# Performance work log

Hardware: AMD Instinct MI355X
Metric: run time of the kernel (lower is better)

Reference implementation:

```python
import jax, jax.numpy as jnp
import numpy as np
import math

N, C, E, K_TOP = 4096, 256, 131072, 32
NEG_SLOPE = 0.2  # GATConv default negative_slope


def _mlp(x, w1, b1, w2, b2):
    # Linear -> relu -> Linear (dropout is identity in eval mode)
    return jax.nn.relu(x @ w1 + b1) @ w2 + b2


def _gat_alpha(x, w, a_src, a_dst, src, dst, n):
    # PyG GATConv attention coefficients (heads=1), softmax over incoming edges per dst
    h = x @ w                                                   # [N,C]
    logits = jax.nn.leaky_relu((h @ a_src)[src] + (h @ a_dst)[dst], NEG_SLOPE)  # [E]
    m = jnp.full((n,), -jnp.inf, dtype=logits.dtype).at[dst].max(logits)
    e = jnp.exp(logits - m[dst])
    s = jax.ops.segment_sum(e, dst, num_segments=n)
    return e / s[dst]                                           # [E]


def _mha_w(x, wq, bq, wk, bk):
    # nn.MultiheadAttention attention weights, heads=1, unbatched [N,C] input
    q = x @ wq + bq
    k = x @ wk + bk
    return jax.nn.softmax((q @ k.T) * (1.0 / math.sqrt(C)), axis=-1)  # [N,N]


def _forward(ae, pe, se,
             ae_w1, ae_b1, ae_w2, ae_b2,
             pe_w1, pe_b1, pe_w2, pe_b2,
             se_w1, se_b1, se_w2, se_b2,
             ae_gw, ae_as, ae_ad,
             pe_gw, pe_as, pe_ad,
             se_gw, se_as, se_ad,
             ae_wq, ae_bq, ae_wk, ae_bk,
             pe_wq, pe_bq, pe_wk, pe_bk,
             se_wq, se_bq, se_wk, se_bk,
             a_l, b_l, c_l, a_g, b_g, c_g,
             w_local, w_global,
             edge_index, K):
    n = ae.shape[0]
    ae = _mlp(ae, ae_w1, ae_b1, ae_w2, ae_b2)
    pe = _mlp(pe, pe_w1, pe_b1, pe_w2, pe_b2)
    se = _mlp(se, se_w1, se_b1, se_w2, se_b2)

    src, dst = edge_index[0], edge_index[1]

    # ---- local branch: fused GAT attention coeffs -> weighted mean aggregation ----
    pa = _gat_alpha(pe, pe_gw, pe_as, pe_ad, src, dst, n)
    sa = _gat_alpha(se, se_gw, se_as, se_ad, src, dst, n)
    aa = _gat_alpha(ae, ae_gw, ae_as, ae_ad, src, dst, n)
    local_attn = a_l * pa + b_l * sa + c_l * aa                 # [E]
    msg = local_attn[:, None] * ae[src]                         # [E,C]
    summ = jax.ops.segment_sum(msg, dst, num_segments=n)
    cnt = jax.ops.segment_sum(jnp.ones((src.shape[0],), msg.dtype), dst, num_segments=n)
    out_local = summ / jnp.maximum(cnt, 1.0)[:, None]           # mean aggr

    # ---- global branch: dense self-attn maps + adj masking + per-column top-K ----
    pw = _mha_w(pe, pe_wq, pe_bq, pe_wk, pe_bk)                 # [N,N]
    sw = _mha_w(se, se_wq, se_bq, se_wk, se_bk)
    aw = _mha_w(ae, ae_wq, ae_bq, ae_wk, ae_bk)
    sample_attn = a_g * pw + b_g * sw
    adj = jnp.zeros((n, n), sample_attn.dtype).at[src, dst].add(1.0)
    sample_attn = jnp.where(adj > 0, jnp.zeros((), sample_attn.dtype), sample_attn)
    # torch topk(dim=1) on [1,N,N] == top-K along axis 0 (per column) of [N,N]
    _, idx = jax.lax.top_k(sample_attn.T, K)                    # [N,K] row indices per column
    maskT = jnp.zeros((n, n), sample_attn.dtype).at[jnp.arange(n)[:, None], idx].set(1.0)
    mask = maskT.T
    g_attn = (0.5 * a_g + 0.5 * b_g) * (sample_attn * mask) + c_g * (aw * mask)
    col = jnp.sum(g_attn, axis=0)                               # column sums (torch dim=1 on [1,N,N])
    g_attn = g_attn / col[None, :]
    out_global = g_attn @ ae                                    # [N,C]

    return out_local @ w_local + out_global @ w_global


def setup_inputs() -> dict:
    key = jax.random.key(0)
    it = iter(jax.random.split(key, 64))
    g = lambda shape, s=0.06: jax.random.normal(next(it), shape, dtype=jnp.float32) * s
    inp = {"ae": g((N, C), 1.0), "pe": g((N, C), 1.0), "se": g((N, C), 1.0)}
    for p in ("ae", "pe", "se"):
        inp[p + "_w1"] = g((C, 2 * C)); inp[p + "_b1"] = jnp.zeros((2 * C,), jnp.float32)
        inp[p + "_w2"] = g((2 * C, C)); inp[p + "_b2"] = jnp.zeros((C,), jnp.float32)
        inp[p + "_gw"] = g((C, C)); inp[p + "_as"] = g((C,)); inp[p + "_ad"] = g((C,))
        inp[p + "_wq"] = g((C, C)); inp[p + "_bq"] = jnp.zeros((C,), jnp.float32)
        inp[p + "_wk"] = g((C, C)); inp[p + "_bk"] = jnp.zeros((C,), jnp.float32)
    for s in ("a_l", "b_l", "c_l", "a_g", "b_g", "c_g"):
        inp[s] = jnp.float32(0.33)
    inp["w_local"] = g((C, C))
    inp["w_global"] = g((C, C))
    inp["edge_index"] = jax.random.randint(next(it), (2, E), 0, N, dtype=jnp.int32)
    inp["K"] = K_TOP
    return inp


def reference(ae, pe, se,
              ae_w1, ae_b1, ae_w2, ae_b2,
              pe_w1, pe_b1, pe_w2, pe_b2,
              se_w1, se_b1, se_w2, se_b2,
              ae_gw, ae_as, ae_ad,
              pe_gw, pe_as, pe_ad,
              se_gw, se_as, se_ad,
              ae_wq, ae_bq, ae_wk, ae_bk,
              pe_wq, pe_bq, pe_wk, pe_bk,
              se_wq, se_bq, se_wk, se_bk,
              a_l, b_l, c_l, a_g, b_g, c_g,
              w_local, w_global,
              edge_index, K):
    return _forward(ae, pe, se,
                    ae_w1, ae_b1, ae_w2, ae_b2,
                    pe_w1, pe_b1, pe_w2, pe_b2,
                    se_w1, se_b1, se_w2, se_b2,
                    ae_gw, ae_as, ae_ad,
                    pe_gw, pe_as, pe_ad,
                    se_gw, se_as, se_ad,
                    ae_wq, ae_bq, ae_wk, ae_bk,
                    pe_wq, pe_bq, pe_wk, pe_bk,
                    se_wq, se_bq, se_wk, se_bk,
                    a_l, b_l, c_l, a_g, b_g, c_g,
                    w_local, w_global,
                    edge_index, K)
```

## Files before the change

kernel.cpp:

```cpp
#include <hip/hip_runtime.h>

#define NN 4096
#define CC 256
#define EE 131072
#define KT 32

typedef unsigned short ushort_t;
typedef __attribute__((ext_vector_type(8))) short short8;
typedef __attribute__((ext_vector_type(4))) float float4v;

__device__ __forceinline__ ushort_t f2bf(float x) {
    union { float f; unsigned u; } a; a.f = x;
    unsigned r = (a.u + 0x7FFF + ((a.u >> 16) & 1)) >> 16;
    return (ushort_t)r;
}
__device__ __forceinline__ float bf2f(ushort_t b) {
    union { float f; unsigned u; } a; a.u = ((unsigned)b) << 16;
    return a.f;
}

constexpr size_t OFF_EPT  = 0;
constexpr size_t OFF_EST  = OFF_EPT + 16777216;
constexpr size_t OFF_SEG  = OFF_EST + 16777216;
constexpr size_t OFF_LP   = OFF_SEG + 12288;
constexpr size_t OFF_LS   = OFF_LP + 4096;
constexpr size_t OFF_LA   = OFF_LS + 4096;
constexpr size_t OFF_ECNT = OFF_LA + 4096;
constexpr size_t OFF_GCNT = OFF_ECNT + 4096;
constexpr size_t OFF_ADJ  = OFF_GCNT + 4096;
constexpr size_t ZERO_END = OFF_ADJ + 524288;
constexpr size_t OFF_XM   = ZERO_END;
constexpr size_t OFF_QK   = OFF_XM + 3*1048576;
constexpr size_t OFF_WEXP = OFF_QK + 6*1048576;
constexpr size_t OFF_HS   = OFF_WEXP + 3*131072;
constexpr size_t OFF_HD   = OFF_HS + 12288;
constexpr size_t OFF_WSD  = OFF_HD + 12288;
constexpr size_t OFF_TKI  = OFF_WSD + 1536;
constexpr size_t OFF_TKV  = OFF_TKI + 131072;
constexpr size_t OFF_GN   = OFF_TKV + 131072;
constexpr size_t OFF_EOFF = OFF_GN + 131072;
constexpr size_t OFF_ECUR = OFF_EOFF + 4097;
constexpr size_t OFF_ELST = OFF_ECUR + 4096;
constexpr size_t OFF_GOFF = OFF_ELST + 131072;
constexpr size_t OFF_GCUR = OFF_GOFF + 4097;
constexpr size_t OFF_GLST = OFF_GCUR + 4096;
constexpr size_t OFF_WLT  = OFF_GLST + 131072;
constexpr size_t WS_FLOATS = OFF_WLT + 131072;

constexpr size_t SH_XINH = 0;
constexpr size_t SH_XINL = 3145728;
constexpr size_t SH_HIDH = 6291456;
constexpr size_t SH_HIDL = 12582912;
constexpr size_t SH_XMH  = 18874368;
constexpr size_t SH_XML  = 22020096;
constexpr size_t SH_WT   = 25165824;
constexpr size_t WT_BR   = 786432;

struct TArgs {
    const float* s[14]; ushort_t* h[14]; ushort_t* l[14];
    int nshift[14]; int total[14]; int kstride[14]; int koff[14];
};

__global__ __launch_bounds__(256)
void wtrans_k(TArgs a)
{
    int z = blockIdx.z;
    int idx = blockIdx.x * 256 + threadIdx.x;
    if (idx >= a.total[z]) return;
    int n = idx & ((1 << a.nshift[z]) - 1);
    int k = idx >> a.nshift[z];
    float v = a.s[z][idx];
    ushort_t hh = f2bf(v);
    size_t o = (size_t)n * a.kstride[z] + a.koff[z] + k;
    a.h[z][o] = hh;
    a.l[z][o] = f2bf(v - bf2f(hh));
}

__global__ __launch_bounds__(256)
void split3_k(const float* s0, const float* s1, const float* s2,
              ushort_t* hb, ushort_t* lb, size_t nper)
{
    int z = blockIdx.z;
    const float* s = (z == 0) ? s0 : (z == 1) ? s1 : s2;
    ushort_t* h = hb + (size_t)z * nper;
    ushort_t* l = lb + (size_t)z * nper;
    size_t i = (size_t)(blockIdx.x * 256 + threadIdx.x) * 4;
    float4 v = *(const float4*)(s + i);
    ushort_t h0 = f2bf(v.x), h1 = f2bf(v.y), h2 = f2bf(v.z), h3 = f2bf(v.w);
    ushort_t l0 = f2bf(v.x - bf2f(h0)), l1 = f2bf(v.y - bf2f(h1));
    ushort_t l2 = f2bf(v.z - bf2f(h2)), l3 = f2bf(v.w - bf2f(h3));
    uint2 hw, lw;
    hw.x = (unsigned)h0 | ((unsigned)h1 << 16); hw.y = (unsigned)h2 | ((unsigned)h3 << 16);
    lw.x = (unsigned)l0 | ((unsigned)l1 << 16); lw.y = (unsigned)l2 | ((unsigned)l3 << 16);
    *(uint2*)(h + i) = hw;
    *(uint2*)(l + i) = lw;
}

struct MArgs {
    const ushort_t* Ah[6]; const ushort_t* Al[6];
    const ushort_t* Bh[6]; const ushort_t* Bl[6];
    const float* bias[6];
    float* Cf[6]; ushort_t* Ch[6]; ushort_t* Cl[6];
};

template<int RELU>
__global__ __launch_bounds__(256)
void mgemm_k(MArgs a, int N, int K)
{
    __shared__ ushort_t SA[2][64 * 32];
    __shared__ ushort_t SB[2][64 * 32];

    const int z = blockIdx.z;
    const int t = threadIdx.x, wave = t >> 6, lane = t & 63;
    const int wi = wave & 1, wj = wave >> 1;
    const int lrow = lane & 15, lquad = lane >> 4;

    const ushort_t* src = (wave == 0) ? a.Ah[z] : (wave == 1) ? a.Al[z]
                        : (wave == 2) ? a.Bh[z] : a.Bl[z];
    ushort_t* dst = (wave == 0) ? &SA[0][0] : (wave == 1) ? &SA[1][0]
                  : (wave == 2) ? &SB[0][0] : &SB[1][0];
    const int rbase = ((wave < 2) ? blockIdx.x : blockIdx.y) * 64;
    const int sr = lane >> 2, sq = lane & 3;

    float4v acc[2][2] = {};

    for (int k0 = 0; k0 < K; k0 += 32) {
        #pragma unroll
        for (int it = 0; it < 4; ++it) {
            const ushort_t* g = src + (size_t)(rbase + it * 16 + sr) * K + k0 + sq * 8;
            __builtin_amdgcn_global_load_lds(
                (const __attribute__((address_space(1))) void*)g,
                (__attribute__((address_space(3))) void*)(dst + it * 512),
                16, 0, 0);
        }
        __syncthreads();

        short8 fAh[2], fAl[2], fBh[2], fBl[2];
        #pragma unroll
        for (int mt = 0; mt < 2; ++mt) {
            int ra = wi * 32 + mt * 16 + lrow;
            fAh[mt] = *(const short8*)&SA[0][ra * 32 + lquad * 8];
            fAl[mt] = *(const short8*)&SA[1][ra * 32 + lquad * 8];
        }
        #pragma unroll
        for (int nt = 0; nt < 2; ++nt) {
            int rb = wj * 32 + nt * 16 + lrow;
            fBh[nt] = *(const short8*)&SB[0][rb * 32 + lquad * 8];
            fBl[nt] = *(const short8*)&SB[1][rb * 32 + lquad * 8];
        }
        #pragma unroll
        for (int mt = 0; mt < 2; ++mt)
            #pragma unroll
            for (int nt = 0; nt < 2; ++nt) {
                acc[mt][nt] = __builtin_amdgcn_mfma_f32_16x16x32_bf16(fAh[mt], fBh[nt], acc[mt][nt], 0, 0, 0);
                acc[mt][nt] = __builtin_amdgcn_mfma_f32_16x16x32_bf16(fAh[mt], fBl[nt], acc[mt][nt], 0, 0, 0);
                acc[mt][nt] = __builtin_amdgcn_mfma_f32_16x16x32_bf16(fAl[mt], fBh[nt], acc[mt][nt], 0, 0, 0);
            }
        __syncthreads();
    }

    const float* bias = a.bias[z];
    float* Cf = a.Cf[z];
    ushort_t* Ch = a.Ch[z]; ushort_t* Cl = a.Cl[z];
    const int i0w = blockIdx.x * 64 + wi * 32, j0w = blockIdx.y * 64 + wj * 32;
    #pragma unroll
    for (int mt = 0; mt < 2; ++mt) {
        const int ib = i0w + mt * 16 + lquad * 4;
        #pragma unroll
        for (int nt = 0; nt < 2; ++nt) {
            const int j = j0w + nt * 16 + lrow;
            float bj = bias ? bias[j] : 0.f;
            #pragma unroll
            for (int r = 0; r < 4; ++r) {
                float v = acc[mt][nt][r] + bj;
                if (RELU) v = fmaxf(v, 0.f);
                if (Cf) Cf[(size_t)(ib + r) * N + j] = v;
                if (Ch) {
                    ushort_t h = f2bf(v);
                    Ch[(size_t)(ib + r) * N + j] = h;
                    Cl[(size_t)(ib + r) * N + j] = f2bf(v - bf2f(h));
                }
            }
        }
    }
}

struct QArgs {
    const ushort_t* qh[3]; const ushort_t* ql[3];
    const ushort_t* kh[3]; const ushort_t* kl[3];
    float* ept[3]; float* rs[3];
};

__global__ __launch_bounds__(256)
void qk_mfma_k(QArgs a, float scale)
{
    __shared__ ushort_t SA[2][128 * 32];
    __shared__ ushort_t SB[2][128 * 32];

    const int z = blockIdx.z;
    const int t = threadIdx.x;
    const int wave = t >> 6, lane = t & 63;
    const int wi = wave & 1, wj = wave >> 1;
    const int i0w = blockIdx.x * 128 + wi * 64;
    const int j0w = blockIdx.y * 128 + wj * 64;
    const int lrow = lane & 15, lquad = lane >> 4;

    const ushort_t* src = (wave == 0) ? a.qh[z] : (wave == 1) ? a.ql[z]
                        : (wave == 2) ? a.kh[z] : a.kl[z];
    ushort_t* dst = (wave == 0) ? &SA[0][0] : (wave == 1) ? &SA[1][0]
                  : (wave == 2) ? &SB[0][0] : &SB[1][0];
    const int rbase = (wave < 2) ? blockIdx.x * 128 : blockIdx.y * 128;
    const int sr = lane >> 2, sq = lane & 3;

    float4v acc[4][4] = {};

    for (int k0 = 0; k0 < CC; k0 += 32) {
        #pragma unroll
        for (int it = 0; it < 8; ++it) {
            const ushort_t* g = src + (size_t)(rbase + it * 16 + sr) * CC + k0 + sq * 8;
            __builtin_amdgcn_global_load_lds(
                (const __attribute__((address_space(1))) void*)g,
                (__attribute__((address_space(3))) void*)(dst + it * 512),
                16, 0, 0);
        }
        __syncthreads();

        short8 Ah[4], Al[4], Bh[4], Bl[4];
        #pragma unroll
        for (int mt = 0; mt < 4; ++mt) {
            int ra = wi * 64 + mt * 16 + lrow;
            Ah[mt] = *(const short8*)&SA[0][ra * 32 + lquad * 8];
            Al[mt] = *(const short8*)&SA[1][ra * 32 + lquad * 8];
        }
        #pragma unroll
        for (int nt = 0; nt < 4; ++nt) {
            int rb = wj * 64 + nt * 16 + lrow;
            Bh[nt] = *(const short8*)&SB[0][rb * 32 + lquad * 8];
            Bl[nt] = *(const short8*)&SB[1][rb * 32 + lquad * 8];
        }
        #pragma unroll
        for (int mt = 0; mt < 4; ++mt)
            #pragma unroll
            for (int nt = 0; nt < 4; ++nt) {
                acc[mt][nt] = __builtin_amdgcn_mfma_f32_16x16x32_bf16(Ah[mt], Bh[nt], acc[mt][nt], 0, 0, 0);
                acc[mt][nt] = __builtin_amdgcn_mfma_f32_16x16x32_bf16(Ah[mt], Bl[nt], acc[mt][nt], 0, 0, 0);
                acc[mt][nt] = __builtin_amdgcn_mfma_f32_16x16x32_bf16(Al[mt], Bh[nt], acc[mt][nt], 0, 0, 0);
            }
        __syncthreads();
    }

    float* ept = a.ept[z];
    float* rowsum = a.rs[z];
    #pragma unroll
    for (int mt = 0; mt < 4; ++mt) {
        const int ib = i0w + mt * 16 + lquad * 4;
        float part[4] = {0.f, 0.f, 0.f, 0.f};
        #pragma unroll
        for (int nt = 0; nt < 4; ++nt) {
            const int j = j0w + nt * 16 + lrow;
            float e0 = expf(acc[mt][nt][0] * scale);
            float e1 = expf(acc[mt][nt][1] * scale);
            float e2 = expf(acc[mt][nt][2] * scale);
            float e3 = expf(acc[mt][nt][3] * scale);
            part[0] += e0; part[1] += e1; part[2] += e2; part[3] += e3;
            if (ept)
                *(float4*)&ept[(size_t)j * NN + ib] = make_float4(e0, e1, e2, e3);
        }
        #pragma unroll
        for (int r = 0; r < 4; ++r) {
            float p = part[r];
            p += __shfl_xor(p, 1, 64);
            p += __shfl_xor(p, 2, 64);
            p += __shfl_xor(p, 4, 64);
            p += __shfl_xor(p, 8, 64);
            if (lrow == 0) atomicAdd(&rowsum[ib + r], p);
        }
    }
}

__global__ void invrows_k(float* __restrict__ lp, float* __restrict__ ls,
                          const float* agp, const float* bgp)
{
    int i = blockIdx.x * 256 + threadIdx.x;
    lp[i] = (*agp) / lp[i];
    ls[i] = (*bgp) / ls[i];
}

__global__ __launch_bounds__(256)
void gatvec_k(const float* g0, const float* g1, const float* g2,
              const float* v0, const float* v1, const float* v2,
              const float* v3, const float* v4, const float* v5,
              float* __restrict__ wsd)
{
    int b = blockIdx.x;
    const float* gw = (b < 2) ? g0 : (b < 4) ? g1 : g2;
    const float* av = (b == 0) ? v0 : (b == 1) ? v1 : (b == 2) ? v2
                    : (b == 3) ? v3 : (b == 4) ? v4 : v5;
    int tdx = threadIdx.x;
    float s = 0.f;
    for (int c = 0; c < CC; ++c) s += gw[(size_t)tdx * CC + c] * av[c];
    wsd[b * 256 + tdx] = s;
}

__global__ __launch_bounds__(256)
void hshd_k(const float* __restrict__ Xp, const float* __restrict__ Xs,
            const float* __restrict__ Xa, const float* __restrict__ wsd,
            float* __restrict__ hs, float* __restrict__ hd)
{
    int b = blockIdx.y, row = blockIdx.x, t = threadIdx.x;
    const float* X = (b == 0) ? Xp : (b == 1) ? Xs : Xa;
    float x = X[(size_t)row * CC + t];
    float p1 = x * wsd[b * 512 + t];
    float p2 = x * wsd[b * 512 + 256 + t];
    for (int off = 32; off; off >>= 1) {
        p1 += __shfl_down(p1, off, 64);
        p2 += __shfl_down(p2, off, 64);
    }
    __shared__ float s1[4], s2[4];
    if ((t & 63) == 0) { s1[t >> 6] = p1; s2[t >> 6] = p2; }
    __syncthreads();
    if (t == 0) {
        hs[b * NN + row] = s1[0] + s1[1] + s1[2] + s1[3];
        hd[b * NN + row] = s2[0] + s2[1] + s2[2] + s2[3];
    }
}

__global__ __launch_bounds__(256)
void edge_k(const int* __restrict__ ei, const float* __restrict__ hs,
            const float* __restrict__ hd, float* __restrict__ wexp,
            float* __restrict__ seg, unsigned* __restrict__ bits,
            int* __restrict__ cnt)
{
    int e = blockIdx.x * 256 + threadIdx.x;
    int s = ei[e], d = ei[EE + e];
    #pragma unroll
    for (int b = 0; b < 3; ++b) {
        float l = hs[b * NN + s] + hd[b * NN + d];
        l = (l > 0.f) ? l : 0.2f * l;
        float w = expf(l);
        wexp[(size_t)b * EE + e] = w;
        atomicAdd(&seg[b * NN + d], w);
    }
    size_t lin = (size_t)d * NN + s;
    atomicOr(&bits[lin >> 5], 1u << (lin & 31));
    atomicAdd(&cnt[d], 1);
}

__global__ void gcount_k(const int* __restrict__ tki, int* __restrict__ cnt)
{
    int p = blockIdx.x * 256 + threadIdx.x;
    atomicAdd(&cnt[tki[p]], 1);
}

__global__ __launch_bounds__(256)
void prefix_k(const int* __restrict__ cnt, int* __restrict__ off, int* __restrict__ cur)
{
    __shared__ int part[257];
    int t = threadIdx.x;
    int loc[16]; int s = 0;
    #pragma unroll
    for (int u = 0; u < 16; ++u) { loc[u] = s; s += cnt[t * 16 + u]; }
    part[t + 1] = s;
    if (t == 0) part[0] = 0;
    __syncthreads();
    if (t == 0) for (int i = 1; i <= 256; ++i) part[i] += part[i - 1];
    __syncthreads();
    int b = part[t];
    #pragma unroll
    for (int u = 0; u < 16; ++u) { off[t * 16 + u] = b + loc[u]; cur[t * 16 + u] = b + loc[u]; }
    if (t == 255) off[4096] = part[256];
}

__global__ void efill_k(const int* __restrict__ ei, int* __restrict__ cur,
                        int* __restrict__ lst)
{
    int e = blockIdx.x * 256 + threadIdx.x;
    int p = atomicAdd(&cur[ei[EE + e]], 1);
    lst[p] = e;
}

__global__ void gfill_k(const int* __restrict__ tki, int* __restrict__ cur,
                        int* __restrict__ lst)
{
    int p = blockIdx.x * 256 + threadIdx.x;
    int q = atomicAdd(&cur[tki[p]], 1);
    lst[q] = p;
}

__global__ __launch_bounds__(256)
void topk_k(const float* __restrict__ EPT, const float* __restrict__ EST,
            const float* __restrict__ ivp, const float* __restrict__ ivs,
            const unsigned* __restrict__ adjbits,
            int* __restrict__ tki, float* __restrict__ tkv)
{
    __shared__ unsigned lst[4][KT];
    const int j = blockIdx.x, t = threadIdx.x;
    const int w = t >> 6, lane = t & 63;
    const size_t base = (size_t)j * NN;

    unsigned keys[16], kmax = 0;
    #pragma unroll
    for (int u = 0; u < 16; ++u) {
        int i = w * 1024 + u * 64 + lane;
        float v = EPT[base + i] * ivp[i] + EST[base + i] * ivs[i];
        if ((adjbits[(base + i) >> 5] >> (i & 31)) & 1u) v = 0.f;
        union { float f; unsigned u32; } cv; cv.f = v;
        unsigned k = (cv.u32 & 0xFFFFFC00u) | (unsigned)(1023 - (i & 1023));
        keys[u] = k;
        kmax = k > kmax ? k : kmax;
    }

    for (int r = 0; r < KT; ++r) {
        unsigned k = kmax;
        #pragma unroll
        for (int off = 1; off < 64; off <<= 1) {
            unsigned o = __shfl_xor(k, off, 64);
            k = o > k ? o : k;
        }
        if (lane == 0) lst[w][r] = k;
        if (kmax == k) {
            kmax = 0;
            #pragma unroll
            for (int u = 0; u < 16; ++u) {
                if (keys[u] == k) keys[u] = 0;
                kmax = keys[u] > kmax ? keys[u] : kmax;
            }
        }
    }
    __syncthreads();

    if (t == 0) {
        unsigned h0 = lst[0][0], h1 = lst[1][0], h2 = lst[2][0], h3 = lst[3][0];
        int p0 = 0, p1 = 0, p2 = 0, p3 = 0;
        for (int r = 0; r < KT; ++r) {
            unsigned m01 = h0 > h1 ? h0 : h1;
            unsigned m23 = h2 > h3 ? h2 : h3;
            unsigned m = m01 > m23 ? m01 : m23;
            int wsel;
            if      (m == h0) { wsel = 0; ++p0; h0 = (p0 < KT) ? lst[0][p0] : 0; }
            else if (m == h1) { wsel = 1; ++p1; h1 = (p1 < KT) ? lst[1][p1] : 0; }
            else if (m == h2) { wsel = 2; ++p2; h2 = (p2 < KT) ? lst[2][p2] : 0; }
            else              { wsel = 3; ++p3; h3 = (p3 < KT) ? lst[3][p3] : 0; }
            union { unsigned u32; float f; } cv; cv.u32 = m & 0xFFFFFC00u;
            tkv[j * KT + r] = cv.f;
            tki[j * KT + r] = wsel * 1024 + 1023 - (int)(m & 0x3FFu);
        }
    }
}

__global__ __launch_bounds__(256)
void awcol_k(const ushort_t* __restrict__ qh, const ushort_t* __restrict__ ql,
             const ushort_t* __restrict__ kh, const ushort_t* __restrict__ kl,
             const float* __restrict__ La, const int* __restrict__ tki,
             const float* __restrict__ tkv,
             const float* agp, const float* bgp, const float* cgp,
             float* __restrict__ gn)
{
    __shared__ float kj[CC];
    __shared__ float gv[KT];
    __shared__ float cs_sh;
    int j = blockIdx.x, t = threadIdx.x;
    kj[t] = bf2f(kh[(size_t)j * CC + t]) + bf2f(kl[(size_t)j * CC + t]);
    __syncthreads();
    float hg = 0.5f * (*agp) + 0.5f * (*bgp), cg = *cgp;
    int wv = t >> 6, ln = t & 63;
    for (int k = wv; k < KT; k += 4) {
        int i = tki[j * KT + k];
        float p = 0.f;
        #pragma unroll
        for (int u = 0; u < 4; ++u) {
            int c = ln + u * 64;
            float q = bf2f(qh[(size_t)i * CC + c]) + bf2f(ql[(size_t)i * CC + c]);
            p += q * kj[c];
        }
        for (int off = 32; off; off >>= 1) p += __shfl_down(p, off, 64);
        if (ln == 0) {
            float aw = expf(p * 0.0625f) / La[i];
            gv[k] = hg * tkv[j * KT + k] + cg * aw;
        }
    }
    __syncthreads();
    if (t == 0) { float cs = 0.f; for (int k = 0; k < KT; ++k) cs += gv[k]; cs_sh = cs; }
    __syncthreads();
    if (t < KT) gn[j * KT + t] = gv[t] / cs_sh;
}

__global__ __launch_bounds__(256)
void lgather_k(const int* __restrict__ ei, const int* __restrict__ eoff,
               const int* __restrict__ elst,
               const float* __restrict__ wexp, const float* __restrict__ seg,
               const float* __restrict__ aem,
               const float* alp, const float* blp, const float* clp,
               ushort_t* __restrict__ outch, ushort_t* __restrict__ outcl)
{
    int wv = threadIdx.x >> 6, ln = threadIdx.x & 63;
    int d = blockIdx.x * 4 + wv;
    int beg = eoff[d], end = eoff[d + 1];
    float i0 = (*alp) / seg[d];
    float i1 = (*blp) / seg[NN + d];
    float i2 = (*clp) / seg[2 * NN + d];
    float4 acc = {0.f, 0.f, 0.f, 0.f};
    for (int c = beg; c < end; c += 64) {
        int n = min(64, end - c);
        int s = 0; float la = 0.f;
        if (ln < n) {
            int e = elst[c + ln];
            s = ei[e];
            la = i0 * wexp[e] + i1 * wexp[EE + e] + i2 * wexp[2 * (size_t)EE + e];
        }
        for (int u = 0; u < n; ++u) {
            float lau = __shfl(la, u, 64);
            int   su  = __shfl(s, u, 64);
            const float4 v = *(const float4*)&aem[(size_t)su * CC + ln * 4];
            acc.x += lau * v.x; acc.y += lau * v.y;
            acc.z += lau * v.z; acc.w += lau * v.w;
        }
    }
    float inv = 1.f / fmaxf((float)(end - beg), 1.f);
    acc.x *= inv; acc.y *= inv; acc.z *= inv; acc.w *= inv;
    ushort_t h0 = f2bf(acc.x), h1 = f2bf(acc.y), h2 = f2bf(acc.z), h3 = f2bf(acc.w);
    uint2 hw, lw;
    hw.x = (unsigned)h0 | ((unsigned)h1 << 16); hw.y = (unsigned)h2 | ((unsigned)h3 << 16);
    lw.x = (unsigned)f2bf(acc.x - bf2f(h0)) | ((unsigned)f2bf(acc.y - bf2f(h1)) << 16);
    lw.y = (unsigned)f2bf(acc.z - bf2f(h2)) | ((unsigned)f2bf(acc.w - bf2f(h3)) << 16);
    *(uint2*)&outch[(size_t)d * 512 + ln * 4] = hw;
    *(uint2*)&outcl[(size_t)d * 512 + ln * 4] = lw;
}

__global__ __launch_bounds__(256)
void ggather_k(const int* __restrict__ goff, const int* __restrict__ glst,
               const float* __restrict__ gn, const float* __restrict__ aem,
               ushort_t* __restrict__ outch, ushort_t* __restrict__ outcl)
{
    int wv = threadIdx.x >> 6, ln = threadIdx.x & 63;
    int i = blockIdx.x * 4 + wv;
    int beg = goff[i], end = goff[i + 1];
    float4 acc = {0.f, 0.f, 0.f, 0.f};
    for (int c = beg; c < end; c += 64) {
        int n = min(64, end - c);
        int j = 0; float g = 0.f;
        if (ln < n) {
            int p = glst[c + ln];
            j = p >> 5;
            g = gn[p];
        }
        for (int u = 0; u < n; ++u) {
            float gu = __shfl(g, u, 64);
            int   ju = __shfl(j, u, 64);
            const float4 v = *(const float4*)&aem[(size_t)ju * CC + ln * 4];
            acc.x += gu * v.x; acc.y += gu * v.y;
            acc.z += gu * v.z; acc.w += gu * v.w;
        }
    }
    ushort_t h0 = f2bf(acc.x), h1 = f2bf(acc.y), h2 = f2bf(acc.z), h3 = f2bf(acc.w);
    uint2 hw, lw;
    hw.x = (unsigned)h0 | ((unsigned)h1 << 16); hw.y = (unsigned)h2 | ((unsigned)h3 << 16);
    lw.x = (unsigned)f2bf(acc.x - bf2f(h0)) | ((unsigned)f2bf(acc.y - bf2f(h1)) << 16);
    lw.y = (unsigned)f2bf(acc.z - bf2f(h2)) | ((unsigned)f2bf(acc.w - bf2f(h3)) << 16);
    *(uint2*)&outch[(size_t)i * 512 + 256 + ln * 4] = hw;
    *(uint2*)&outcl[(size_t)i * 512 + 256 + ln * 4] = lw;
}

__global__ void diag_k(float* out, float v) { out[0] = v; }

extern "C" void kernel_launch(void* const* d_in, const int* in_sizes, int n_in,
                              void* d_out, int out_size, void* d_ws, size_t ws_size,
                              hipStream_t stream)
{
    (void)in_sizes; (void)n_in; (void)out_size;

    if (ws_size < WS_FLOATS * sizeof(float)) {
        diag_k<<<1, 1, 0, stream>>>((float*)d_out, (float)(ws_size >> 20));
        return;
    }

    float* W = (float*)d_ws;
    float* EPT = W + OFF_EPT;  float* EST = W + OFF_EST;
    float* SEG = W + OFF_SEG;
    float* LP = W + OFF_LP;    float* LS = W + OFF_LS;   float* LA = W + OFF_LA;
    int* ECNT = (int*)(W + OFF_ECNT);
    int* GCNT = (int*)(W + OFF_GCNT);
    unsigned* ADJ = (unsigned*)(W + OFF_ADJ);
    float* XM = W + OFF_XM;
    ushort_t* QKS = (ushort_t*)(W + OFF_QK);
    float* WEXP = W + OFF_WEXP;
    float* HS = W + OFF_HS;    float* HD = W + OFF_HD;   float* WSD = W + OFF_WSD;
    int*   TKI = (int*)(W + OFF_TKI);
    float* TKV = W + OFF_TKV;  float* GN = W + OFF_GN;
    int* EOFF = (int*)(W + OFF_EOFF); int* ECUR = (int*)(W + OFF_ECUR);
    int* ELST = (int*)(W + OFF_ELST);
    int* GOFF = (int*)(W + OFF_GOFF); int* GCUR = (int*)(W + OFF_GCUR);
    int* GLST = (int*)(W + OFF_GLST);

    ushort_t* PRO = (ushort_t*)EPT;
    ushort_t* EPI = (ushort_t*)EST;
    ushort_t* WLT = (ushort_t*)(W + OFF_WLT);

    ushort_t* XINH = PRO + SH_XINH; ushort_t* XINL = PRO + SH_XINL;
    ushort_t* HIDH = PRO + SH_HIDH; ushort_t* HIDL = PRO + SH_HIDL;
    ushort_t* XMH  = PRO + SH_XMH;  ushort_t* XML  = PRO + SH_XML;

    auto W1T = [&](int b, int hl) { return PRO + SH_WT + (size_t)b * WT_BR + hl * 131072; };
    auto W2T = [&](int b, int hl) { return PRO + SH_WT + (size_t)b * WT_BR + 262144 + hl * 131072; };
    auto WQT = [&](int b, int hl) { return PRO + SH_WT + (size_t)b * WT_BR + 524288 + hl * 65536; };
    auto WKT = [&](int b, int hl) { return PRO + SH_WT + (size_t)b * WT_BR + 655360 + hl * 65536; };
    ushort_t* WCT_H = WLT;
    ushort_t* WCT_L = WLT + 131072;
    ushort_t* OUTCH = EPI;
    ushort_t* OUTCL = EPI + 2097152;

    auto QHp = [&](int b) { return QKS + (size_t)(b * 4 + 0) * 1048576; };
    auto QLp = [&](int b) { return QKS + (size_t)(b * 4 + 1) * 1048576; };
    auto KHp = [&](int b) { return QKS + (size_t)(b * 4 + 2) * 1048576; };
    auto KLp = [&](int b) { return QKS + (size_t)(b * 4 + 3) * 1048576; };

    const float* Xin[3] = {(const float*)d_in[1], (const float*)d_in[2], (const float*)d_in[0]};
    const int base_idx[3] = {14, 25, 3};
    const float *w1[3], *b1[3], *w2[3], *b2[3], *gw[3], *asv[3], *adv[3], *wq[3], *bq[3], *wk[3], *bk[3];
    for (int b = 0; b < 3; ++b) {
        int o = base_idx[b];
        w1[b] = (const float*)d_in[o + 0]; b1[b] = (const float*)d_in[o + 1];
        w2[b] = (const float*)d_in[o + 2]; b2[b] = (const float*)d_in[o + 3];
        gw[b] = (const float*)d_in[o + 4]; asv[b] = (const float*)d_in[o + 5];
        adv[b] = (const float*)d_in[o + 6];
        wq[b] = (const float*)d_in[o + 7]; bq[b] = (const float*)d_in[o + 8];
        wk[b] = (const float*)d_in[o + 9]; bk[b] = (const float*)d_in[o + 10];
    }
    const float* al = (const float*)d_in[36]; const float* bl = (const float*)d_in[37];
    const float* cl = (const float*)d_in[38];
    const float* ag = (const float*)d_in[39]; const float* bg = (const float*)d_in[40];
    const float* cg = (const float*)d_in[41];
    const float* wloc = (const float*)d_in[42];
    const float* wglb = (const float*)d_in[43];
    const int* ei = (const int*)d_in[44];

    dim3 blk(256);

    hipMemsetAsync(SEG, 0, (ZERO_END - OFF_SEG) * sizeof(float), stream);

    {
        TArgs a{};
        for (int b = 0; b < 3; ++b) {
            a.s[b] = w1[b]; a.h[b] = W1T(b, 0); a.l[b] = W1T(b, 1);
            a.nshift[b] = 9; a.total[b] = 131072; a.kstride[b] = 256; a.koff[b] = 0;
            a.s[3 + b] = w2[b]; a.h[3 + b] = W2T(b, 0); a.l[3 + b] = W2T(b, 1);
            a.nshift[3 + b] = 8; a.total[3 + b] = 131072; a.kstride[3 + b] = 512; a.koff[3 + b] = 0;
            a.s[6 + b] = wq[b]; a.h[6 + b] = WQT(b, 0); a.l[6 + b] = WQT(b, 1);
            a.nshift[6 + b] = 8; a.total[6 + b] = 65536; a.kstride[6 + b] = 256; a.koff[6 + b] = 0;
            a.s[9 + b] = wk[b]; a.h[9 + b] = WKT(b, 0); a.l[9 + b] = WKT(b, 1);
            a.nshift[9 + b] = 8; a.total[9 + b] = 65536; a.kstride[9 + b] = 256; a.koff[9 + b] = 0;
        }
        a.s[12] = wloc; a.h[12] = WCT_H; a.l[12] = WCT_L;
        a.nshift[12] = 8; a.total[12] = 65536; a.kstride[12] = 512; a.koff[12] = 0;
        a.s[13] = wglb; a.h[13] = WCT_H; a.l[13] = WCT_L;
        a.nshift[13] = 8; a.total[13] = 65536; a.kstride[13] = 512; a.koff[13] = 256;
        wtrans_k<<<dim3(512, 1, 14), blk, 0, stream>>>(a);
    }

    split3_k<<<dim3(1024, 1, 3), blk, 0, stream>>>(Xin[0], Xin[1], Xin[2], XINH, XINL, 1048576);

    {
        MArgs a{};
        for (int b = 0; b < 3; ++b) {
            a.Ah[b] = XINH + (size_t)b * 1048576; a.Al[b] = XINL + (size_t)b * 1048576;
            a.Bh[b] = W1T(b, 0); a.Bl[b] = W1T(b, 1); a.bias[b] = b1[b];
            a.Cf[b] = nullptr;
            a.Ch[b] = HIDH + (size_t)b * 2097152; a.Cl[b] = HIDL + (size_t)b * 2097152;
        }
        mgemm_k<1><<<dim3(64, 8, 3), blk, 0, stream>>>(a, 512, 256);
    }
    {
        MArgs a{};
        for (int b = 0; b < 3; ++b) {
            a.Ah[b] = HIDH + (size_t)b * 2097152; a.Al[b] = HIDL + (size_t)b * 2097152;
            a.Bh[b] = W2T(b, 0); a.Bl[b] = W2T(b, 1); a.bias[b] = b2[b];
            a.Cf[b] = XM + (size_t)b * 1048576;
            a.Ch[b] = XMH + (size_t)b * 1048576; a.Cl[b] = XML + (size_t)b * 1048576;
        }
        mgemm_k<0><<<dim3(64, 4, 3), blk, 0, stream>>>(a, 256, 512);
    }

    gatvec_k<<<6, blk, 0, stream>>>(gw[0], gw[1], gw[2],
                                    asv[0], adv[0], asv[1], adv[1], asv[2], adv[2], WSD);
    hshd_k<<<dim3(NN, 3), blk, 0, stream>>>(XM, XM + 1048576, XM + 2 * 1048576, WSD, HS, HD);
    edge_k<<<EE / 256, blk, 0, stream>>>(ei, HS, HD, WEXP, SEG, ADJ, ECNT);

    prefix_k<<<1, blk, 0, stream>>>(ECNT, EOFF, ECUR);
    efill_k<<<EE / 256, blk, 0, stream>>>(ei, ECUR, ELST);

    {
        MArgs a{};
        for (int b = 0; b < 3; ++b) {
            a.Ah[b] = XMH + (size_t)b * 1048576; a.Al[b] = XML + (size_t)b * 1048576;
            a.Bh[b] = WQT(b, 0); a.Bl[b] = WQT(b, 1); a.bias[b] = bq[b];
            a.Cf[b] = nullptr; a.Ch[b] = QHp(b); a.Cl[b] = QLp(b);
            a.Ah[3 + b] = a.Ah[b]; a.Al[3 + b] = a.Al[b];
            a.Bh[3 + b] = WKT(b, 0); a.Bl[3 + b] = WKT(b, 1); a.bias[3 + b] = bk[b];
            a.Cf[3 + b] = nullptr; a.Ch[3 + b] = KHp(b); a.Cl[3 + b] = KLp(b);
        }
        mgemm_k<0><<<dim3(64, 4, 6), blk, 0, stream>>>(a, 256, 256);
    }

    {
        QArgs a{};
        for (int b = 0; b < 3; ++b) {
            a.qh[b] = QHp(b); a.ql[b] = QLp(b); a.kh[b] = KHp(b); a.kl[b] = KLp(b);
        }
        a.ept[0] = EPT; a.rs[0] = LP;
        a.ept[1] = EST; a.rs[1] = LS;
        a.ept[2] = nullptr; a.rs[2] = LA;
        qk_mfma_k<<<dim3(32, 32, 3), blk, 0, stream>>>(a, 0.0625f);
    }

    invrows_k<<<16, blk, 0, stream>>>(LP, LS, ag, bg);

    topk_k<<<NN, blk, 0, stream>>>(EPT, EST, LP, LS, ADJ, TKI, TKV);

    gcount_k<<<(NN * KT) / 256, blk, 0, stream>>>(TKI, GCNT);
    prefix_k<<<1, blk, 0, stream>>>(GCNT, GOFF, GCUR);
    gfill_k<<<(NN * KT) / 256, blk, 0, stream>>>(TKI, GCUR, GLST);

    awcol_k<<<NN, blk, 0, stream>>>(QHp(2), QLp(2), KHp(2), KLp(2), LA,
                                    TKI, TKV, ag, bg, cg, GN);

    lgather_k<<<NN / 4, blk, 0, stream>>>(ei, EOFF, ELST, WEXP, SEG,
                                          XM + 2 * 1048576, al, bl, cl, OUTCH, OUTCL);
    ggather_k<<<NN / 4, blk, 0, stream>>>(GOFF, GLST, GN, XM + 2 * 1048576, OUTCH, OUTCL);

    {
        MArgs a{};
        a.Ah[0] = OUTCH; a.Al[0] = OUTCL;
        a.Bh[0] = WCT_H; a.Bl[0] = WCT_L; a.bias[0] = nullptr;
        a.Cf[0] = (float*)d_out; a.Ch[0] = nullptr; a.Cl[0] = nullptr;
        mgemm_k<0><<<dim3(64, 4, 1), blk, 0, stream>>>(a, 256, 512);
    }
}
```

Baseline: 602.5 us.

## Swizzle LDS tiles in MFMA GEMMs and compute GAT softmax sums in gather

Adds an XOR swizzle on the 16-byte column chunks of the LDS tiles in both the generic MFMA GEMM and the QK GEMM, applied on the global-to-LDS load address and on the fragment reads, to avoid LDS bank conflicts. It also drops the per-edge float atomicAdd into the segment-sum buffer in edge_k. Each destination's softmax denominators are instead reduced inside lgather_k by walking its CSR edge list and doing a wave shuffle reduction. This removes 3×E atomics and a memset region, at the cost of an extra pass over wexp per destination in the gather.

```diff
diff --git a/kernel.cpp b/kernel.cpp
--- a/kernel.cpp
+++ b/kernel.cpp
@@ -21,8 +21,7 @@
 
 constexpr size_t OFF_EPT  = 0;
 constexpr size_t OFF_EST  = OFF_EPT + 16777216;
-constexpr size_t OFF_SEG  = OFF_EST + 16777216;
-constexpr size_t OFF_LP   = OFF_SEG + 12288;
+constexpr size_t OFF_LP   = OFF_EST + 16777216;
 constexpr size_t OFF_LS   = OFF_LP + 4096;
 constexpr size_t OFF_LA   = OFF_LS + 4096;
 constexpr size_t OFF_ECNT = OFF_LA + 4096;
@@ -121,13 +120,14 @@
                   : (wave == 2) ? &SB[0][0] : &SB[1][0];
     const int rbase = ((wave < 2) ? blockIdx.x : blockIdx.y) * 64;
     const int sr = lane >> 2, sq = lane & 3;
+    const int gsq = sq ^ ((sr >> 1) & 3);
 
     float4v acc[2][2] = {};
 
     for (int k0 = 0; k0 < K; k0 += 32) {
         #pragma unroll
         for (int it = 0; it < 4; ++it) {
-            const ushort_t* g = src + (size_t)(rbase + it * 16 + sr) * K + k0 + sq * 8;
+            const ushort_t* g = src + (size_t)(rbase + it * 16 + sr) * K + k0 + gsq * 8;
             __builtin_amdgcn_global_load_lds(
                 (const __attribute__((address_space(1))) void*)g,
                 (__attribute__((address_space(3))) void*)(dst + it * 512),
@@ -139,14 +139,16 @@
         #pragma unroll
         for (int mt = 0; mt < 2; ++mt) {
             int ra = wi * 32 + mt * 16 + lrow;
-            fAh[mt] = *(const short8*)&SA[0][ra * 32 + lquad * 8];
-            fAl[mt] = *(const short8*)&SA[1][ra * 32 + lquad * 8];
+            int ca = (lquad ^ ((ra >> 1) & 3)) * 8;
+            fAh[mt] = *(const short8*)&SA[0][ra * 32 + ca];
+            fAl[mt] = *(const short8*)&SA[1][ra * 32 + ca];
         }
         #pragma unroll
         for (int nt = 0; nt < 2; ++nt) {
             int rb = wj * 32 + nt * 16 + lrow;
-            fBh[nt] = *(const short8*)&SB[0][rb * 32 + lquad * 8];
-            fBl[nt] = *(const short8*)&SB[1][rb * 32 + lquad * 8];
+            int cb = (lquad ^ ((rb >> 1) & 3)) * 8;
+            fBh[nt] = *(const short8*)&SB[0][rb * 32 + cb];
+            fBl[nt] = *(const short8*)&SB[1][rb * 32 + cb];
         }
         #pragma unroll
         for (int mt = 0; mt < 2; ++mt)
@@ -211,13 +213,14 @@
                   : (wave == 2) ? &SB[0][0] : &SB[1][0];
     const int rbase = (wave < 2) ? blockIdx.x * 128 : blockIdx.y * 128;
     const int sr = lane >> 2, sq = lane & 3;
+    const int gsq = sq ^ ((sr >> 1) & 3);
 
     float4v acc[4][4] = {};
 
     for (int k0 = 0; k0 < CC; k0 += 32) {
         #pragma unroll
         for (int it = 0; it < 8; ++it) {
-            const ushort_t* g = src + (size_t)(rbase + it * 16 + sr) * CC + k0 + sq * 8;
+            const ushort_t* g = src + (size_t)(rbase + it * 16 + sr) * CC + k0 + gsq * 8;
             __builtin_amdgcn_global_load_lds(
                 (const __attribute__((address_space(1))) void*)g,
                 (__attribute__((address_space(3))) void*)(dst + it * 512),
@@ -229,14 +232,16 @@
         #pragma unroll
         for (int mt = 0; mt < 4; ++mt) {
             int ra = wi * 64 + mt * 16 + lrow;
-            Ah[mt] = *(const short8*)&SA[0][ra * 32 + lquad * 8];
-            Al[mt] = *(const short8*)&SA[1][ra * 32 + lquad * 8];
+            int ca = (lquad ^ ((ra >> 1) & 3)) * 8;
+            Ah[mt] = *(const short8*)&SA[0][ra * 32 + ca];
+            Al[mt] = *(const short8*)&SA[1][ra * 32 + ca];
         }
         #pragma unroll
         for (int nt = 0; nt < 4; ++nt) {
             int rb = wj * 64 + nt * 16 + lrow;
-            Bh[nt] = *(const short8*)&SB[0][rb * 32 + lquad * 8];
-            Bl[nt] = *(const short8*)&SB[1][rb * 32 + lquad * 8];
+            int cb = (lquad ^ ((rb >> 1) & 3)) * 8;
+            Bh[nt] = *(const short8*)&SB[0][rb * 32 + cb];
+            Bl[nt] = *(const short8*)&SB[1][rb * 32 + cb];
         }
         #pragma unroll
         for (int mt = 0; mt < 4; ++mt)
@@ -328,8 +333,7 @@
 __global__ __launch_bounds__(256)
 void edge_k(const int* __restrict__ ei, const float* __restrict__ hs,
             const float* __restrict__ hd, float* __restrict__ wexp,
-            float* __restrict__ seg, unsigned* __restrict__ bits,
-            int* __restrict__ cnt)
+            unsigned* __restrict__ bits, int* __restrict__ cnt)
 {
     int e = blockIdx.x * 256 + threadIdx.x;
     int s = ei[e], d = ei[EE + e];
@@ -337,9 +341,7 @@
     for (int b = 0; b < 3; ++b) {
         float l = hs[b * NN + s] + hd[b * NN + d];
         l = (l > 0.f) ? l : 0.2f * l;
-        float w = expf(l);
-        wexp[(size_t)b * EE + e] = w;
-        atomicAdd(&seg[b * NN + d], w);
+        wexp[(size_t)b * EE + e] = expf(l);
     }
     size_t lin = (size_t)d * NN + s;
     atomicOr(&bits[lin >> 5], 1u << (lin & 31));
@@ -488,7 +490,7 @@
 __global__ __launch_bounds__(256)
 void lgather_k(const int* __restrict__ ei, const int* __restrict__ eoff,
                const int* __restrict__ elst,
-               const float* __restrict__ wexp, const float* __restrict__ seg,
+               const float* __restrict__ wexp,
                const float* __restrict__ aem,
                const float* alp, const float* blp, const float* clp,
                ushort_t* __restrict__ outch, ushort_t* __restrict__ outcl)
@@ -496,9 +498,22 @@
     int wv = threadIdx.x >> 6, ln = threadIdx.x & 63;
     int d = blockIdx.x * 4 + wv;
     int beg = eoff[d], end = eoff[d + 1];
-    float i0 = (*alp) / seg[d];
-    float i1 = (*blp) / seg[NN + d];
-    float i2 = (*clp) / seg[2 * NN + d];
+
+    float s1 = 0.f, s2 = 0.f, s3 = 0.f;
+    for (int c = beg + ln; c < end; c += 64) {
+        int e = elst[c];
+        s1 += wexp[e];
+        s2 += wexp[EE + e];
+        s3 += wexp[2 * (size_t)EE + e];
+    }
+    #pragma unroll
+    for (int off = 1; off < 64; off <<= 1) {
+        s1 += __shfl_xor(s1, off, 64);
+        s2 += __shfl_xor(s2, off, 64);
+        s3 += __shfl_xor(s3, off, 64);
+    }
+    float i0 = (*alp) / s1, i1 = (*blp) / s2, i2 = (*clp) / s3;
+
     float4 acc = {0.f, 0.f, 0.f, 0.f};
     for (int c = beg; c < end; c += 64) {
         int n = min(64, end - c);
@@ -576,7 +591,6 @@
 
     float* W = (float*)d_ws;
     float* EPT = W + OFF_EPT;  float* EST = W + OFF_EST;
-    float* SEG = W + OFF_SEG;
     float* LP = W + OFF_LP;    float* LS = W + OFF_LS;   float* LA = W + OFF_LA;
     int* ECNT = (int*)(W + OFF_ECNT);
     int* GCNT = (int*)(W + OFF_GCNT);
@@ -636,7 +650,7 @@
 
     dim3 blk(256);
 
-    hipMemsetAsync(SEG, 0, (ZERO_END - OFF_SEG) * sizeof(float), stream);
+    hipMemsetAsync(LP, 0, (ZERO_END - OFF_LP) * sizeof(float), stream);
 
     {
         TArgs a{};
@@ -683,7 +697,7 @@
     gatvec_k<<<6, blk, 0, stream>>>(gw[0], gw[1], gw[2],
                                     asv[0], adv[0], asv[1], adv[1], asv[2], adv[2], WSD);
     hshd_k<<<dim3(NN, 3), blk, 0, stream>>>(XM, XM + 1048576, XM + 2 * 1048576, WSD, HS, HD);
-    edge_k<<<EE / 256, blk, 0, stream>>>(ei, HS, HD, WEXP, SEG, ADJ, ECNT);
+    edge_k<<<EE / 256, blk, 0, stream>>>(ei, HS, HD, WEXP, ADJ, ECNT);
 
     prefix_k<<<1, blk, 0, stream>>>(ECNT, EOFF, ECUR);
     efill_k<<<EE / 256, blk, 0, stream>>>(ei, ECUR, ELST);
@@ -723,7 +737,7 @@
     awcol_k<<<NN, blk, 0, stream>>>(QHp(2), QLp(2), KHp(2), KLp(2), LA,
                                     TKI, TKV, ag, bg, cg, GN);
 
-    lgather_k<<<NN / 4, blk, 0, stream>>>(ei, EOFF, ELST, WEXP, SEG,
+    lgather_k<<<NN / 4, blk, 0, stream>>>(ei, EOFF, ELST, WEXP,
                                           XM + 2 * 1048576, al, bl, cl, OUTCH, OUTCL);
     ggather_k<<<NN / 4, blk, 0, stream>>>(GOFF, GLST, GN, XM + 2 * 1048576, OUTCH, OUTCL);
 
```

New measurement: 568.7 us. -5.6%, faster.
